# Performance work log

Measured on AMD Instinct MI355X. Metric: run time of the kernel, lower is better.

## Reference

```python
import jax, jax.numpy as jnp
import numpy as np


def setup_inputs() -> dict:
    key = jax.random.key(0)
    kL, kx = jax.random.split(key)
    N, D, K = 4096, 256, 8
    L = jax.random.normal(kL, (N, N), dtype=jnp.float32)
    x = jax.random.normal(kx, (N, D), dtype=jnp.float32)
    # Taylor-like decaying filter coefficients (fixed, non-trained in the original)
    coeffs = jnp.asarray([1.0, 0.9, 0.45, 0.15, 0.0375, 0.0075, 0.00125, 0.000179],
                         dtype=jnp.float32)
    return {"L": L, "x": x, "coeffs": coeffs}


def reference(L, x, coeffs):
    """filter = sum_i coeffs[i] * L^i ; out = filter @ x.

    Same math as torch.stack([c*L.matrix_power(i)]).sum(0) @ x, but the powers
    are built with a single running product instead of K independent
    matrix_power calls.
    """
    N = L.shape[0]
    K = coeffs.shape[0]
    P = jnp.eye(N, dtype=L.dtype)          # L^0
    filt = coeffs[0] * P
    for i in range(1, K):                   # small fixed polynomial order
        P = P @ L                            # L^i
        filt = filt + coeffs[i] * P
    return filt @ x                          # [N, D]
```

## Files before the change

kernel.cpp:

```cpp
#include <hip/hip_runtime.h>
#include <hip/hip_bf16.h>

#define NDIM 4096
#define DDIM 256
#define KORD 8

#define BM 128
#define BN 128
#define BK 32
#define SPLITK 8
#define KSLICE (NDIM / SPLITK)
#define NSTEP (KSLICE / BK)
#define ELEMS (NDIM * DDIM)

#define LBUF 16384

typedef __attribute__((ext_vector_type(8))) short bf16x8;
typedef __attribute__((ext_vector_type(4))) float f32x4;

__device__ __forceinline__ ushort f2bf(float v) {
    __hip_bfloat16 h = __float2bfloat16(v);
    return *reinterpret_cast<ushort*>(&h);
}
__device__ __forceinline__ float bf2f(ushort u) {
    __hip_bfloat16 h = *reinterpret_cast<__hip_bfloat16*>(&u);
    return __bfloat162float(h);
}
__device__ __forceinline__ void split2(float v, ushort& h, ushort& l) {
    h = f2bf(v);
    l = f2bf(v - bf2f(h));
}
__device__ __forceinline__ uint4 pack8(const ushort* s) {
    uint4 r;
    r.x = (uint)s[0] | ((uint)s[1] << 16);
    r.y = (uint)s[2] | ((uint)s[3] << 16);
    r.z = (uint)s[4] | ((uint)s[5] << 16);
    r.w = (uint)s[6] | ((uint)s[7] << 16);
    return r;
}

__global__ __launch_bounds__(256)
void split_L(const float* __restrict__ L, ushort* __restrict__ Lhi,
             ushort* __restrict__ Llo)
{
    const int e0 = (blockIdx.x * 256 + threadIdx.x) * 8;
    float4 a = *(const float4*)&L[e0];
    float4 b = *(const float4*)&L[e0 + 4];
    float v[8] = {a.x, a.y, a.z, a.w, b.x, b.y, b.z, b.w};
    ushort h[8], l[8];
#pragma unroll
    for (int j = 0; j < 8; ++j) split2(v[j], h[j], l[j]);
    *(uint4*)&Lhi[e0] = pack8(h);
    *(uint4*)&Llo[e0] = pack8(l);
}

__global__ __launch_bounds__(256)
void split_x(const float* __restrict__ x, const float* __restrict__ coeffs,
             ushort* __restrict__ yhiT, ushort* __restrict__ yloT)
{
    __shared__ float tile[64][65];
    const float c = coeffs[KORD - 1];
    const int m0 = blockIdx.x * 64, n0 = blockIdx.y * 64;
    const int t = threadIdx.x;
    const int ml = t >> 2, n4 = (t & 3) * 16;
#pragma unroll
    for (int j = 0; j < 4; ++j) {
        float4 v = *(const float4*)&x[(size_t)(m0 + ml) * DDIM + n0 + n4 + j * 4];
        tile[ml][n4 + j * 4 + 0] = c * v.x;
        tile[ml][n4 + j * 4 + 1] = c * v.y;
        tile[ml][n4 + j * 4 + 2] = c * v.z;
        tile[ml][n4 + j * 4 + 3] = c * v.w;
    }
    __syncthreads();
    const int nl = t >> 2, m16 = (t & 3) * 16;
    ushort h[16], l[16];
#pragma unroll
    for (int j = 0; j < 16; ++j) split2(tile[m16 + j][nl], h[j], l[j]);
    const size_t ob = (size_t)(n0 + nl) * NDIM + m0 + m16;
    *(uint4*)&yhiT[ob]     = pack8(h);
    *(uint4*)&yhiT[ob + 8] = pack8(h + 8);
    *(uint4*)&yloT[ob]     = pack8(l);
    *(uint4*)&yloT[ob + 8] = pack8(l + 8);
}

__global__ __launch_bounds__(256, 2)
void gemm_fused(const ushort* __restrict__ Lhi, const ushort* __restrict__ Llo,
                const ushort* __restrict__ yhiT, const ushort* __restrict__ yloT,
                float* __restrict__ P)
{
    __shared__ ushort lds[2 * LBUF];

    const int bid  = blockIdx.x;
    const int z    = bid & 7;
    const int slot = bid >> 3;
    const int nt   = slot & 1;
    const int mt   = slot >> 1;

    const int m0 = mt * BM, n0 = nt * BN;
    const int kb = z * KSLICE;

    const int t = threadIdx.x;
    const int lane = t & 63, wid = t >> 6;
    const int wr = wid >> 1, wc = wid & 1;

    const int rowS = t >> 2;
    const int ksw  = ((t & 3) ^ (rowS & 3)) * 8;
    const ushort* sAh = Lhi  + (size_t)(m0 + rowS) * NDIM + kb + ksw;
    const ushort* sAl = Llo  + (size_t)(m0 + rowS) * NDIM + kb + ksw;
    const ushort* sBh = yhiT + (size_t)(n0 + rowS) * NDIM + kb + ksw;
    const ushort* sBl = yloT + (size_t)(n0 + rowS) * NDIM + kb + ksw;
    const size_t R64 = (size_t)64 * NDIM;
    const int wb = wid * 512;

#define GLD(src, dstoff)                                                     \
    __builtin_amdgcn_global_load_lds(                                        \
        (const __attribute__((address_space(1))) uint*)(src),                \
        (__attribute__((address_space(3))) uint*)(&lds[dstoff]), 16, 0, 0)

#define STAGE(buf, ko)                                                       \
    do {                                                                     \
        const int _b = (buf) * LBUF;                                         \
        GLD(sAh + (ko),        _b + wb);                                     \
        GLD(sAh + (ko) + R64,  _b + 2048 + wb);                              \
        GLD(sAl + (ko),        _b + 4096 + wb);                              \
        GLD(sAl + (ko) + R64,  _b + 6144 + wb);                              \
        GLD(sBh + (ko),        _b + 8192 + wb);                              \
        GLD(sBh + (ko) + R64,  _b + 10240 + wb);                             \
        GLD(sBl + (ko),        _b + 12288 + wb);                             \
        GLD(sBl + (ko) + R64,  _b + 14336 + wb);                             \
    } while (0)

    const int frow = lane & 15;
    const int fsw  = (((lane >> 4) ^ (frow & 3))) * 8;
    const int arB  = (wr * 64 + frow) * 32 + fsw;
    const int brB  = (wc * 64 + frow) * 32 + fsw;

    f32x4 acc[4][4];
#pragma unroll
    for (int i = 0; i < 4; ++i)
#pragma unroll
        for (int j = 0; j < 4; ++j) acc[i][j] = (f32x4){0.f, 0.f, 0.f, 0.f};

    STAGE(0, 0);
    STAGE(1, BK);

    for (int step = 0; step < NSTEP; ++step) {
        if (step + 1 < NSTEP)
            asm volatile("s_waitcnt vmcnt(8)" ::: "memory");
        else
            asm volatile("s_waitcnt vmcnt(0)" ::: "memory");
        __builtin_amdgcn_sched_barrier(0);
        __builtin_amdgcn_s_barrier();
        __builtin_amdgcn_sched_barrier(0);

        const int b = (step & 1) * LBUF;
        bf16x8 ah[4], al[4], bh[4], bl[4];
#pragma unroll
        for (int i = 0; i < 4; ++i) {
            ah[i] = *(const bf16x8*)&lds[b + arB + i * 512];
            al[i] = *(const bf16x8*)&lds[b + arB + i * 512 + 4096];
        }
#pragma unroll
        for (int j = 0; j < 4; ++j) {
            bh[j] = *(const bf16x8*)&lds[b + brB + j * 512 + 8192];
            bl[j] = *(const bf16x8*)&lds[b + brB + j * 512 + 12288];
        }
        asm volatile("s_waitcnt lgkmcnt(0)" ::: "memory");
        __builtin_amdgcn_sched_barrier(0);
        __builtin_amdgcn_s_barrier();
        __builtin_amdgcn_sched_barrier(0);

        if (step + 2 < NSTEP) STAGE(step & 1, (step + 2) * BK);

        __builtin_amdgcn_s_setprio(1);
#pragma unroll
        for (int i = 0; i < 4; ++i)
#pragma unroll
            for (int j = 0; j < 4; ++j) {
                acc[i][j] = __builtin_amdgcn_mfma_f32_16x16x32_bf16(
                    ah[i], bh[j], acc[i][j], 0, 0, 0);
                acc[i][j] = __builtin_amdgcn_mfma_f32_16x16x32_bf16(
                    ah[i], bl[j], acc[i][j], 0, 0, 0);
                acc[i][j] = __builtin_amdgcn_mfma_f32_16x16x32_bf16(
                    al[i], bh[j], acc[i][j], 0, 0, 0);
            }
        __builtin_amdgcn_s_setprio(0);
    }
#undef STAGE
#undef GLD

    float* Pp = P + (size_t)z * ELEMS;
    const int crow = (lane >> 4) * 4;
    const int ccol = lane & 15;
#pragma unroll
    for (int i = 0; i < 4; ++i)
#pragma unroll
        for (int j = 0; j < 4; ++j)
#pragma unroll
            for (int r = 0; r < 4; ++r)
                Pp[(size_t)(m0 + wr * 64 + i * 16 + crow + r) * DDIM
                   + n0 + wc * 64 + j * 16 + ccol] = acc[i][j][r];
}

__global__ __launch_bounds__(256)
void combine(const float* __restrict__ P, const float* __restrict__ x,
             const float* __restrict__ coeffs, const int ci, const int last,
             ushort* __restrict__ yhiT, ushort* __restrict__ yloT,
             float* __restrict__ out)
{
    __shared__ float tile[64][65];
    const float c = coeffs[ci];
    const int m0 = blockIdx.x * 64, n0 = blockIdx.y * 64;
    const int t = threadIdx.x;
    const int ml = t >> 2, n4 = (t & 3) * 16;
    const size_t base = (size_t)(m0 + ml) * DDIM + n0 + n4;
    float acc[16];
#pragma unroll
    for (int j = 0; j < 4; ++j) {
        float4 v = *(const float4*)&x[base + j * 4];
        acc[j * 4 + 0] = c * v.x; acc[j * 4 + 1] = c * v.y;
        acc[j * 4 + 2] = c * v.z; acc[j * 4 + 3] = c * v.w;
    }
#pragma unroll
    for (int s = 0; s < SPLITK; ++s) {
        const float* Pp = P + (size_t)s * ELEMS;
#pragma unroll
        for (int j = 0; j < 4; ++j) {
            float4 v = *(const float4*)&Pp[base + j * 4];
            acc[j * 4 + 0] += v.x; acc[j * 4 + 1] += v.y;
            acc[j * 4 + 2] += v.z; acc[j * 4 + 3] += v.w;
        }
    }
    if (last) {
#pragma unroll
        for (int j = 0; j < 4; ++j) {
            float4 v;
            v.x = acc[j * 4 + 0]; v.y = acc[j * 4 + 1];
            v.z = acc[j * 4 + 2]; v.w = acc[j * 4 + 3];
            *(float4*)&out[base + j * 4] = v;
        }
        return;
    }
#pragma unroll
    for (int j = 0; j < 16; ++j) tile[ml][n4 + j] = acc[j];
    __syncthreads();
    const int nl = t >> 2, m16 = (t & 3) * 16;
    ushort h[16], l[16];
#pragma unroll
    for (int j = 0; j < 16; ++j) split2(tile[m16 + j][nl], h[j], l[j]);
    const size_t ob = (size_t)(n0 + nl) * NDIM + m0 + m16;
    *(uint4*)&yhiT[ob]     = pack8(h);
    *(uint4*)&yhiT[ob + 8] = pack8(h + 8);
    *(uint4*)&yloT[ob]     = pack8(l);
    *(uint4*)&yloT[ob + 8] = pack8(l + 8);
}

extern "C" void kernel_launch(void* const* d_in, const int* in_sizes, int n_in,
                              void* d_out, int out_size, void* d_ws, size_t ws_size,
                              hipStream_t stream)
{
    const float* L      = (const float*)d_in[0];
    const float* x      = (const float*)d_in[1];
    const float* coeffs = (const float*)d_in[2];
    float* out = (float*)d_out;

    char* w = (char*)d_ws;
    ushort* Lhi  = (ushort*)w;
    ushort* Llo  = (ushort*)(w + (size_t)NDIM * NDIM * 2);
    float*  Pp   = (float*)(w + (size_t)NDIM * NDIM * 4);
    ushort* yhiT = (ushort*)(w + (size_t)NDIM * NDIM * 4 + (size_t)SPLITK * ELEMS * 4);
    ushort* yloT = yhiT + (size_t)DDIM * NDIM;

    split_L<<<NDIM * NDIM / (256 * 8), 256, 0, stream>>>(L, Lhi, Llo);
    split_x<<<dim3(NDIM / 64, DDIM / 64), 256, 0, stream>>>(x, coeffs, yhiT, yloT);

    for (int i = KORD - 2; i >= 0; --i) {
        gemm_fused<<<SPLITK * 64, 256, 0, stream>>>(Lhi, Llo, yhiT, yloT, Pp);
        combine<<<dim3(NDIM / 64, DDIM / 64), 256, 0, stream>>>(
            Pp, x, coeffs, i, (i == 0) ? 1 : 0, yhiT, yloT, out);
    }
}
```

Baseline: 320.7 us.

## Widen GEMM tile to cover full D with 512-thread blocks to reuse L tiles

The split-K GEMM now uses a 128x256 tile so each block covers the whole D dimension, with 8 waves per block instead of 4. Each Lhi/Llo row slice is loaded once per block instead of twice, which halves L traffic from global memory. The LDS layout, swizzle pattern and wait counts are adjusted to match. In exchange the block uses more LDS and registers, and there are half as many blocks (256 instead of 512), which may lower occupancy.

```diff
diff --git a/kernel.cpp b/kernel.cpp
--- a/kernel.cpp
+++ b/kernel.cpp
@@ -6,14 +6,14 @@
 #define KORD 8
 
 #define BM 128
-#define BN 128
+#define BN 256
 #define BK 32
 #define SPLITK 8
 #define KSLICE (NDIM / SPLITK)
 #define NSTEP (KSLICE / BK)
 #define ELEMS (NDIM * DDIM)
 
-#define LBUF 16384
+#define LBUF 24576
 
 typedef __attribute__((ext_vector_type(8))) short bf16x8;
 typedef __attribute__((ext_vector_type(4))) float f32x4;
@@ -83,33 +83,30 @@
     *(uint4*)&yloT[ob + 8] = pack8(l + 8);
 }
 
-__global__ __launch_bounds__(256, 2)
+__global__ __launch_bounds__(512, 2)
 void gemm_fused(const ushort* __restrict__ Lhi, const ushort* __restrict__ Llo,
                 const ushort* __restrict__ yhiT, const ushort* __restrict__ yloT,
                 float* __restrict__ P)
 {
     __shared__ ushort lds[2 * LBUF];
 
-    const int bid  = blockIdx.x;
-    const int z    = bid & 7;
-    const int slot = bid >> 3;
-    const int nt   = slot & 1;
-    const int mt   = slot >> 1;
-
-    const int m0 = mt * BM, n0 = nt * BN;
+    const int bid = blockIdx.x;
+    const int z   = bid & 7;
+    const int mt  = bid >> 3;
+    const int m0 = mt * BM;
     const int kb = z * KSLICE;
 
     const int t = threadIdx.x;
     const int lane = t & 63, wid = t >> 6;
-    const int wr = wid >> 1, wc = wid & 1;
+    const int wr = wid >> 2, wc = wid & 3;
 
     const int rowS = t >> 2;
-    const int ksw  = ((t & 3) ^ (rowS & 3)) * 8;
+    const int ksw  = ((t & 3) ^ ((t >> 3) & 3)) * 8;
     const ushort* sAh = Lhi  + (size_t)(m0 + rowS) * NDIM + kb + ksw;
     const ushort* sAl = Llo  + (size_t)(m0 + rowS) * NDIM + kb + ksw;
-    const ushort* sBh = yhiT + (size_t)(n0 + rowS) * NDIM + kb + ksw;
-    const ushort* sBl = yloT + (size_t)(n0 + rowS) * NDIM + kb + ksw;
-    const size_t R64 = (size_t)64 * NDIM;
+    const ushort* sBh = yhiT + (size_t)rowS * NDIM + kb + ksw;
+    const ushort* sBl = yloT + (size_t)rowS * NDIM + kb + ksw;
+    const size_t R128 = (size_t)128 * NDIM;
     const int wb = wid * 512;
 
 #define GLD(src, dstoff)                                                     \
@@ -120,20 +117,18 @@
 #define STAGE(buf, ko)                                                       \
     do {                                                                     \
         const int _b = (buf) * LBUF;                                         \
-        GLD(sAh + (ko),        _b + wb);                                     \
-        GLD(sAh + (ko) + R64,  _b + 2048 + wb);                              \
-        GLD(sAl + (ko),        _b + 4096 + wb);                              \
-        GLD(sAl + (ko) + R64,  _b + 6144 + wb);                              \
-        GLD(sBh + (ko),        _b + 8192 + wb);                              \
-        GLD(sBh + (ko) + R64,  _b + 10240 + wb);                             \
-        GLD(sBl + (ko),        _b + 12288 + wb);                             \
-        GLD(sBl + (ko) + R64,  _b + 14336 + wb);                             \
+        GLD(sAh + (ko),         _b + wb);                                    \
+        GLD(sAl + (ko),         _b + 4096 + wb);                             \
+        GLD(sBh + (ko),         _b + 8192 + wb);                             \
+        GLD(sBh + (ko) + R128,  _b + 12288 + wb);                           \
+        GLD(sBl + (ko),         _b + 16384 + wb);                            \
+        GLD(sBl + (ko) + R128,  _b + 20480 + wb);                           \
     } while (0)
 
     const int frow = lane & 15;
-    const int fsw  = (((lane >> 4) ^ (frow & 3))) * 8;
-    const int arB  = (wr * 64 + frow) * 32 + fsw;
-    const int brB  = (wc * 64 + frow) * 32 + fsw;
+    const int slotx = (((lane >> 4)) ^ ((frow >> 1) & 3)) * 8;
+    const int arB = (wr * 64 + frow) * 32 + slotx;
+    const int brB = 8192 + (wc * 64 + frow) * 32 + slotx;
 
     f32x4 acc[4][4];
 #pragma unroll
@@ -146,7 +141,7 @@
 
     for (int step = 0; step < NSTEP; ++step) {
         if (step + 1 < NSTEP)
-            asm volatile("s_waitcnt vmcnt(8)" ::: "memory");
+            asm volatile("s_waitcnt vmcnt(6)" ::: "memory");
         else
             asm volatile("s_waitcnt vmcnt(0)" ::: "memory");
         __builtin_amdgcn_sched_barrier(0);
@@ -162,8 +157,8 @@
         }
 #pragma unroll
         for (int j = 0; j < 4; ++j) {
-            bh[j] = *(const bf16x8*)&lds[b + brB + j * 512 + 8192];
-            bl[j] = *(const bf16x8*)&lds[b + brB + j * 512 + 12288];
+            bh[j] = *(const bf16x8*)&lds[b + brB + j * 512];
+            bl[j] = *(const bf16x8*)&lds[b + brB + j * 512 + 8192];
         }
         asm volatile("s_waitcnt lgkmcnt(0)" ::: "memory");
         __builtin_amdgcn_sched_barrier(0);
@@ -199,7 +194,7 @@
 #pragma unroll
             for (int r = 0; r < 4; ++r)
                 Pp[(size_t)(m0 + wr * 64 + i * 16 + crow + r) * DDIM
-                   + n0 + wc * 64 + j * 16 + ccol] = acc[i][j][r];
+                   + wc * 64 + j * 16 + ccol] = acc[i][j][r];
 }
 
 __global__ __launch_bounds__(256)
@@ -275,7 +270,7 @@
     split_x<<<dim3(NDIM / 64, DDIM / 64), 256, 0, stream>>>(x, coeffs, yhiT, yloT);
 
     for (int i = KORD - 2; i >= 0; --i) {
-        gemm_fused<<<SPLITK * 64, 256, 0, stream>>>(Lhi, Llo, yhiT, yloT, Pp);
+        gemm_fused<<<SPLITK * (NDIM / BM), 512, 0, stream>>>(Lhi, Llo, yhiT, yloT, Pp);
         combine<<<dim3(NDIM / 64, DDIM / 64), 256, 0, stream>>>(
             Pp, x, coeffs, i, (i == 0) ? 1 : 0, yhiT, yloT, out);
     }
```

After: 332.1 us. +3.6%, slower.

## Replace double-buffered LDS pipeline with single buffer and higher occupancy

Applied to the files above, without the earlier changes.

Removes the two-stage global_load_lds prefetch pipeline and uses a single LDS buffer with plain __syncthreads around each k-step. Halving LDS lets launch bounds ask for three blocks per CU, so latency is hidden by occupancy rather than software prefetch. The LDS swizzle pattern is also changed. The risk is that load latency is exposed within each block, since loads are no longer overlapped with MFMA work.

```diff
diff --git a/kernel.cpp b/kernel.cpp
--- a/kernel.cpp
+++ b/kernel.cpp
@@ -13,7 +13,6 @@
 #define NSTEP (KSLICE / BK)
 #define ELEMS (NDIM * DDIM)
 
-#define LBUF 16384
 
 typedef __attribute__((ext_vector_type(8))) short bf16x8;
 typedef __attribute__((ext_vector_type(4))) float f32x4;
@@ -83,12 +82,12 @@
     *(uint4*)&yloT[ob + 8] = pack8(l + 8);
 }
 
-__global__ __launch_bounds__(256, 2)
+__global__ __launch_bounds__(256, 3)
 void gemm_fused(const ushort* __restrict__ Lhi, const ushort* __restrict__ Llo,
                 const ushort* __restrict__ yhiT, const ushort* __restrict__ yloT,
                 float* __restrict__ P)
 {
-    __shared__ ushort lds[2 * LBUF];
+    __shared__ ushort lds[16384];
 
     const int bid  = blockIdx.x;
     const int z    = bid & 7;
@@ -104,7 +103,7 @@
     const int wr = wid >> 1, wc = wid & 1;
 
     const int rowS = t >> 2;
-    const int ksw  = ((t & 3) ^ (rowS & 3)) * 8;
+    const int ksw  = ((t & 3) ^ ((t >> 3) & 3)) * 8;
     const ushort* sAh = Lhi  + (size_t)(m0 + rowS) * NDIM + kb + ksw;
     const ushort* sAl = Llo  + (size_t)(m0 + rowS) * NDIM + kb + ksw;
     const ushort* sBh = yhiT + (size_t)(n0 + rowS) * NDIM + kb + ksw;
@@ -117,23 +116,10 @@
         (const __attribute__((address_space(1))) uint*)(src),                \
         (__attribute__((address_space(3))) uint*)(&lds[dstoff]), 16, 0, 0)
 
-#define STAGE(buf, ko)                                                       \
-    do {                                                                     \
-        const int _b = (buf) * LBUF;                                         \
-        GLD(sAh + (ko),        _b + wb);                                     \
-        GLD(sAh + (ko) + R64,  _b + 2048 + wb);                              \
-        GLD(sAl + (ko),        _b + 4096 + wb);                              \
-        GLD(sAl + (ko) + R64,  _b + 6144 + wb);                              \
-        GLD(sBh + (ko),        _b + 8192 + wb);                              \
-        GLD(sBh + (ko) + R64,  _b + 10240 + wb);                             \
-        GLD(sBl + (ko),        _b + 12288 + wb);                             \
-        GLD(sBl + (ko) + R64,  _b + 14336 + wb);                             \
-    } while (0)
-
     const int frow = lane & 15;
-    const int fsw  = (((lane >> 4) ^ (frow & 3))) * 8;
+    const int fsw  = ((lane >> 4) ^ ((frow >> 1) & 3)) * 8;
     const int arB  = (wr * 64 + frow) * 32 + fsw;
-    const int brB  = (wc * 64 + frow) * 32 + fsw;
+    const int brB  = 8192 + (wc * 64 + frow) * 32 + fsw;
 
     f32x4 acc[4][4];
 #pragma unroll
@@ -141,38 +127,29 @@
 #pragma unroll
         for (int j = 0; j < 4; ++j) acc[i][j] = (f32x4){0.f, 0.f, 0.f, 0.f};
 
-    STAGE(0, 0);
-    STAGE(1, BK);
-
     for (int step = 0; step < NSTEP; ++step) {
-        if (step + 1 < NSTEP)
-            asm volatile("s_waitcnt vmcnt(8)" ::: "memory");
-        else
-            asm volatile("s_waitcnt vmcnt(0)" ::: "memory");
-        __builtin_amdgcn_sched_barrier(0);
-        __builtin_amdgcn_s_barrier();
-        __builtin_amdgcn_sched_barrier(0);
-
-        const int b = (step & 1) * LBUF;
+        const int ko = step * BK;
+        GLD(sAh + ko,       wb);
+        GLD(sAh + ko + R64, 2048 + wb);
+        GLD(sAl + ko,       4096 + wb);
+        GLD(sAl + ko + R64, 6144 + wb);
+        GLD(sBh + ko,       8192 + wb);
+        GLD(sBh + ko + R64, 10240 + wb);
+        GLD(sBl + ko,       12288 + wb);
+        GLD(sBl + ko + R64, 14336 + wb);
+        __syncthreads();
+
         bf16x8 ah[4], al[4], bh[4], bl[4];
 #pragma unroll
         for (int i = 0; i < 4; ++i) {
-            ah[i] = *(const bf16x8*)&lds[b + arB + i * 512];
-            al[i] = *(const bf16x8*)&lds[b + arB + i * 512 + 4096];
+            ah[i] = *(const bf16x8*)&lds[arB + i * 512];
+            al[i] = *(const bf16x8*)&lds[arB + i * 512 + 4096];
         }
 #pragma unroll
         for (int j = 0; j < 4; ++j) {
-            bh[j] = *(const bf16x8*)&lds[b + brB + j * 512 + 8192];
-            bl[j] = *(const bf16x8*)&lds[b + brB + j * 512 + 12288];
-        }
-        asm volatile("s_waitcnt lgkmcnt(0)" ::: "memory");
-        __builtin_amdgcn_sched_barrier(0);
-        __builtin_amdgcn_s_barrier();
-        __builtin_amdgcn_sched_barrier(0);
-
-        if (step + 2 < NSTEP) STAGE(step & 1, (step + 2) * BK);
-
-        __builtin_amdgcn_s_setprio(1);
+            bh[j] = *(const bf16x8*)&lds[brB + j * 512];
+            bl[j] = *(const bf16x8*)&lds[brB + j * 512 + 4096];
+        }
 #pragma unroll
         for (int i = 0; i < 4; ++i)
 #pragma unroll
@@ -184,9 +161,8 @@
                 acc[i][j] = __builtin_amdgcn_mfma_f32_16x16x32_bf16(
                     al[i], bh[j], acc[i][j], 0, 0, 0);
             }
-        __builtin_amdgcn_s_setprio(0);
-    }
-#undef STAGE
+        __syncthreads();
+    }
 #undef GLD
 
     float* Pp = P + (size_t)z * ELEMS;
```

Measured after the change: 327.4 us. 2.1% more time.
